# Kernel optimization log

Hardware: AMD Instinct MI355X
Metric: run time of the kernel (lower is better)

Reference implementation:

```python
import jax, jax.numpy as jnp
import numpy as np

EPS = 1e-16

def setup_inputs() -> dict:
    key = jax.random.key(0)
    k1, k2, k3, k4, k5, k6 = jax.random.split(key, 6)
    B, S, NT, E = 8, 256, 50, 64
    # sorted event times in [0, 90); horizon T = 100 > all events; all valid (>=0)
    event_times = jnp.sort(jax.random.uniform(k1, (B, S), dtype=jnp.float32) * 90.0, axis=1)
    event_types = jax.random.randint(k2, (B, S), 0, NT)
    # parameters initialized N(0, 0.1) as in _initialize_parameters
    type_embeddings = 0.1 * jax.random.normal(k3, (NT, E), dtype=jnp.float32)
    a = 0.1 * jax.random.normal(k4, (NT, E), dtype=jnp.float32)
    A = 0.1 * jax.random.normal(k5, (NT, NT, E), dtype=jnp.float32)
    P = 0.1 * jax.random.normal(k6, (NT, NT, E), dtype=jnp.float32)
    return {"event_times": event_times, "event_types": event_types, "T": 100,
            "type_embeddings": type_embeddings, "a": a, "A": A, "P": P}

def _hawkes_nll(event_times, event_types, T, emb, a, A, P):
    B, S = event_times.shape
    NT, E = emb.shape
    Tf = jnp.asarray(T, jnp.float32)
    emb_t = emb[event_types]            # (B,S,E) embedding of each event's type
    a_t = a[event_types]                # (B,S,E)
    valid = event_times >= 0.0          # (B,S)

    # ---- log-likelihood: intensity of the observed type at each event time ----
    # pairwise: axis 1 = query event i, axis 2 = history event j (j < i)
    dt = event_times[:, :, None] - event_times[:, None, :]                 # (B,Si,Sj)
    hist_mask = (jnp.arange(S)[:, None] > jnp.arange(S)[None, :])[None]    # (1,Si,Sj): j<i
    # A_pair[b,i,j,e] = A[type_j, type_i, e]; same for P_pair
    A_pair = A[event_types[:, None, :], event_types[:, :, None]]           # (B,Si,Sj,E)
    P_pair = P[event_types[:, None, :], event_types[:, :, None]]
    emb_i = emb_t[:, :, None, :]                                           # (B,Si,1,E)
    emb_j = emb_t[:, None, :, :]                                           # (B,1,Sj,E)
    decay = jnp.exp(-(emb_i * P_pair) * emb_j * dt[..., None])
    contrib = (emb_i * A_pair) * decay * emb_j                             # (B,Si,Sj,E)
    m = jnp.sum(jnp.where(hist_mask[..., None], contrib, 0.0), axis=2)     # (B,Si,E)
    inten = jnp.sum(jax.nn.softplus(emb_t * a_t + m), axis=-1)             # (B,S)
    ll = jnp.sum(jnp.where(valid, jnp.log(inten + EPS), 0.0))

    # ---- integral approximation (as in compute_loss) ----
    # intensity at horizon T for ALL types, using full valid history
    dT = Tf - event_times                                                  # (B,S)
    A_all = A[event_types]                                                 # (B,S,NT,E): A[t_j, t, e]
    P_all = P[event_types]
    decT = jnp.exp(-(emb[None, None] * P_all) * emb_t[:, :, None, :] * dT[:, :, None, None])
    conT = (emb[None, None] * A_all) * decT * emb_t[:, :, None, :]         # (B,S,NT,E)
    m_T = jnp.sum(jnp.where(valid[:, :, None, None], conT, 0.0), axis=1)   # (B,NT,E)
    inten_T = jnp.sum(jax.nn.softplus(emb * a + m_T), axis=(-2, -1))       # (B,)

    base_sum = jnp.sum(jax.nn.softplus(emb * a))                           # empty-history intensity summed over types
    any_valid = jnp.any(valid, axis=1)                                     # (B,)
    last_time = jnp.where(any_valid, jnp.max(jnp.where(valid, event_times, -1e30), axis=1), 0.0)
    first_time = jnp.where(any_valid, jnp.min(jnp.where(valid, event_times, 1e30), axis=1), 0.0)
    integ_b = jnp.where(any_valid,
                        inten_T * (Tf - last_time) + base_sum * first_time,
                        base_sum * Tf)
    integral = jnp.sum(integ_b)
    return -(ll - integral)

def reference(event_times, event_types, T, type_embeddings, a, A, P):
    return _hawkes_nll(event_times, event_types, T, type_embeddings, a, A, P)
```

## Files before the change

### kernel.cpp

```cpp
#include <hip/hip_runtime.h>
#include <math.h>

#define B   8
#define S   256
#define NT  50
#define E   64
#define NTE (NT * E)
#define EPSF 1e-16f

#define NW        8
#define NTHREADS  (64 * NW)
#define LL_BLOCKS (B * S / 2)
#define IN_BLOCKS (B * NT)

__device__ __forceinline__ float softplus(float x) {
    if (x > 20.0f) return x;
    return log1pf(__expf(x));
}

__device__ __forceinline__ float wave_reduce_sum(float v) {
    #pragma unroll
    for (int off = 32; off > 0; off >>= 1)
        v += __shfl_down(v, off, 64);
    return v;
}

__global__ __launch_bounds__(NTHREADS, 8) void main_kernel(
    const float* __restrict__ times, const int* __restrict__ types,
    const int* __restrict__ Tp,
    const float* __restrict__ emb,  const float* __restrict__ a,
    const float* __restrict__ Amat, const float* __restrict__ Pmat,
    float* __restrict__ ws_ll, float* __restrict__ ws_int)
{
    const int tid = threadIdx.x;
    const int e   = tid & 63;
    const int w   = tid >> 6;
    const int bid = blockIdx.x;
    const int b   = bid / (S / 2);

    __shared__ __align__(16) float  s_emb[NTE];
    __shared__ __align__(16) float4 s_ev[S];
    __shared__ float s_part[2][NW][E];
    __shared__ float s_row[2];

    {
        const float4* __restrict__ emb4 = (const float4*)emb;
        float4* s4 = (float4*)s_emb;
        for (int idx = tid; idx < NTE / 4; idx += NTHREADS)
            s4[idx] = emb4[idx];
    }
    for (int j = tid; j < S; j += NTHREADS) {
        const int ty = types[b * S + j];
        s_ev[j] = make_float4(times[b * S + j],
                              __int_as_float(ty * E),
                              __int_as_float(ty * NTE), 0.0f);
    }
    __syncthreads();

    {
        const int ih = bid % (S / 2);
        const int rows[2] = { ih, S - 1 - ih };
        #pragma unroll
        for (int r = 0; r < 2; ++r) {
            const int   i     = rows[r];
            const float t_i   = s_ev[i].x;
            const int   col   = __float_as_int(s_ev[i].y) + e;
            const float negEi = -s_emb[col];

            float macc = 0.0f;
            #pragma unroll 8
            for (int j = w; j < i; j += NW) {
                const float4 ev  = s_ev[j];
                const float  dtj = t_i - ev.x;
                const int   base = __float_as_int(ev.z) + col;
                const float ej   = s_emb[__float_as_int(ev.y) + e];
                const float Pe   = Pmat[base];
                const float Ae   = Amat[base];
                macc = fmaf(Ae * ej, __expf(negEi * Pe * ej * dtj), macc);
            }
            s_part[r][w][e] = macc;
        }
        __syncthreads();
        if (w < 2) {
            const int   i     = rows[w];
            const float t_i   = s_ev[i].x;
            const int   col   = __float_as_int(s_ev[i].y) + e;
            const float emb_i = s_emb[col];
            float mt = 0.0f;
            #pragma unroll
            for (int q = 0; q < NW; ++q) mt += s_part[w][q][e];
            const float sp    = softplus(fmaf(emb_i, mt, emb_i * a[col]));
            const float inten = wave_reduce_sum(sp);
            if (e == 0)
                s_row[w] = (t_i >= 0.0f) ? logf(inten + EPSF) : 0.0f;
        }
        __syncthreads();
        if (tid == 0) ws_ll[bid] = s_row[0] + s_row[1];
    }

    if (bid < IN_BLOCKS) {
        const int b2 = bid / NT;
        const int k  = bid % NT;

        for (int j = tid; j < S; j += NTHREADS) {
            const int ty = types[b2 * S + j];
            s_ev[j] = make_float4(times[b2 * S + j],
                                  __int_as_float(ty * E),
                                  __int_as_float(ty * NTE), 0.0f);
        }
        __syncthreads();

        const float Tf    = (float)(*Tp);
        const int   colk  = k * E + e;
        const float embk  = s_emb[colk];
        const float negEk = -embk;

        float acc = 0.0f;
        #pragma unroll 8
        for (int i = w; i < S; i += NW) {
            const float4 ev  = s_ev[i];
            const float  dT  = Tf - ev.x;
            const int   base = __float_as_int(ev.z) + colk;
            const float et   = s_emb[__float_as_int(ev.y) + e];
            const float c    = Amat[base] * et * __expf(negEk * Pmat[base] * et * dT);
            acc += (ev.x >= 0.0f) ? c : 0.0f;
        }
        s_part[0][w][e] = acc;
        __syncthreads();
        if (w == 0) {
            float mt = 0.0f;
            #pragma unroll
            for (int q = 0; q < NW; ++q) mt += s_part[0][q][e];
            const float sp = softplus(fmaf(embk, mt, embk * a[colk]));
            const float s  = wave_reduce_sum(sp);
            if (e == 0) ws_int[bid] = s;
        }
    }
}

__global__ __launch_bounds__(256) void finalize_kernel(
    const float* __restrict__ times,
    const int* __restrict__ Tp,
    const float* __restrict__ emb, const float* __restrict__ a,
    const float* __restrict__ ws_ll, const float* __restrict__ ws_int,
    float* __restrict__ out)
{
    const int t    = threadIdx.x;
    const int lane = t & 63;
    const int w    = t >> 6;
    const float Tf = (float)(*Tp);

    float llp = 0.0f;
    for (int idx = t; idx < LL_BLOCKS; idx += 256) llp += ws_ll[idx];
    float bs = 0.0f;
    for (int idx = t; idx < NTE; idx += 256) bs += softplus(emb[idx] * a[idx]);

    __shared__ float red[256], red2[256];
    red[t] = llp; red2[t] = bs;

    __shared__ float s_first[B], s_last[B], s_iT[B], s_any[B];
    for (int b = w; b < B; b += 4) {
        float mn = 1e30f, mx = -1e30f;
        #pragma unroll
        for (int q = 0; q < S / 64; ++q) {
            const float tv = times[b * S + q * 64 + lane];
            const bool valid = (tv >= 0.0f);
            mn = fminf(mn, valid ? tv : 1e30f);
            mx = fmaxf(mx, valid ? tv : -1e30f);
        }
        float iv = (lane < NT) ? ws_int[b * NT + lane] : 0.0f;
        #pragma unroll
        for (int off = 32; off > 0; off >>= 1) {
            mn = fminf(mn, __shfl_down(mn, off, 64));
            mx = fmaxf(mx, __shfl_down(mx, off, 64));
            iv += __shfl_down(iv, off, 64);
        }
        if (lane == 0) {
            const bool any_valid = (mn < 1e29f);
            s_any[b]   = any_valid ? 1.0f : 0.0f;
            s_first[b] = any_valid ? mn : 0.0f;
            s_last[b]  = any_valid ? mx : 0.0f;
            s_iT[b]    = iv;
        }
    }
    __syncthreads();

    for (int off = 128; off > 0; off >>= 1) {
        if (t < off) { red[t] += red[t + off]; red2[t] += red2[t + off]; }
        __syncthreads();
    }

    if (t == 0) {
        const float base_sum = red2[0];
        float integral = 0.0f;
        #pragma unroll
        for (int b = 0; b < B; ++b) {
            integral += (s_any[b] > 0.5f)
                ? s_iT[b] * (Tf - s_last[b]) + base_sum * s_first[b]
                : base_sum * Tf;
        }
        out[0] = integral - red[0];
    }
}

extern "C" void kernel_launch(void* const* d_in, const int* in_sizes, int n_in,
                              void* d_out, int out_size, void* d_ws, size_t ws_size,
                              hipStream_t stream) {
    const float* times = (const float*)d_in[0];
    const int*   types = (const int*)d_in[1];
    const int*   Tp    = (const int*)d_in[2];
    const float* emb   = (const float*)d_in[3];
    const float* a     = (const float*)d_in[4];
    const float* Amat  = (const float*)d_in[5];
    const float* Pmat  = (const float*)d_in[6];

    float* ws     = (float*)d_ws;
    float* ws_ll  = ws;
    float* ws_int = ws + LL_BLOCKS;
    float* out    = (float*)d_out;

    main_kernel<<<LL_BLOCKS, NTHREADS, 0, stream>>>(
        times, types, Tp, emb, a, Amat, Pmat, ws_ll, ws_int);
    finalize_kernel<<<1, 256, 0, stream>>>(times, Tp, emb, a, ws_ll, ws_int, out);
}
```

Before: 88.24 us.

## Use persistent 256-block grid with 16 waves, looping over row pairs and tiles

Drops the grid from 1024 blocks to 256 blocks of 1024 threads, so each block handles 4 row pairs and up to 2 integral tiles. This amortizes the per-block load of the embedding table and event data into shared memory across more work. Per-row log values are now written straight to the workspace, and finalize sums twice as many entries. The cost is fewer blocks in flight, lower occupancy per CU, and extra syncs between iterations.

```diff
diff --git a/kernel.cpp b/kernel.cpp
--- a/kernel.cpp
+++ b/kernel.cpp
@@ -8,10 +8,12 @@
 #define NTE (NT * E)
 #define EPSF 1e-16f
 
-#define NW        8
+#define NW        16
 #define NTHREADS  (64 * NW)
-#define LL_BLOCKS (B * S / 2)
-#define IN_BLOCKS (B * NT)
+#define NBLK      256
+#define PAIRS_PB  4
+#define LL_PAIRS  (B * S / 2)
+#define IN_TILES  (B * NT)
 
 __device__ __forceinline__ float softplus(float x) {
     if (x > 20.0f) return x;
@@ -25,23 +27,22 @@
     return v;
 }
 
-__global__ __launch_bounds__(NTHREADS, 8) void main_kernel(
+__global__ __launch_bounds__(NTHREADS, 4) void main_kernel(
     const float* __restrict__ times, const int* __restrict__ types,
     const int* __restrict__ Tp,
     const float* __restrict__ emb,  const float* __restrict__ a,
     const float* __restrict__ Amat, const float* __restrict__ Pmat,
-    float* __restrict__ ws_ll, float* __restrict__ ws_int)
+    float* __restrict__ ws_ll2, float* __restrict__ ws_int)
 {
     const int tid = threadIdx.x;
     const int e   = tid & 63;
     const int w   = tid >> 6;
     const int bid = blockIdx.x;
-    const int b   = bid / (S / 2);
+    const int b   = bid >> 5;
 
     __shared__ __align__(16) float  s_emb[NTE];
     __shared__ __align__(16) float4 s_ev[S];
     __shared__ float s_part[2][NW][E];
-    __shared__ float s_row[2];
 
     {
         const float4* __restrict__ emb4 = (const float4*)emb;
@@ -57,9 +58,11 @@
     }
     __syncthreads();
 
-    {
-        const int ih = bid % (S / 2);
+    for (int pp = 0; pp < PAIRS_PB; ++pp) {
+        const int pair = bid * PAIRS_PB + pp;
+        const int ih   = pair & 127;
         const int rows[2] = { ih, S - 1 - ih };
+
         #pragma unroll
         for (int r = 0; r < 2; ++r) {
             const int   i     = rows[r];
@@ -92,15 +95,17 @@
             const float sp    = softplus(fmaf(emb_i, mt, emb_i * a[col]));
             const float inten = wave_reduce_sum(sp);
             if (e == 0)
-                s_row[w] = (t_i >= 0.0f) ? logf(inten + EPSF) : 0.0f;
-        }
-        __syncthreads();
-        if (tid == 0) ws_ll[bid] = s_row[0] + s_row[1];
-    }
-
-    if (bid < IN_BLOCKS) {
-        const int b2 = bid / NT;
-        const int k  = bid % NT;
+                ws_ll2[pair * 2 + w] = (t_i >= 0.0f) ? logf(inten + EPSF) : 0.0f;
+        }
+        __syncthreads();
+    }
+
+    #pragma unroll
+    for (int tt = 0; tt < 2; ++tt) {
+        const int t = bid + tt * NBLK;
+        if (t >= IN_TILES) break;
+        const int b2 = t / NT;
+        const int k  = t % NT;
 
         for (int j = tid; j < S; j += NTHREADS) {
             const int ty = types[b2 * S + j];
@@ -133,8 +138,9 @@
             for (int q = 0; q < NW; ++q) mt += s_part[0][q][e];
             const float sp = softplus(fmaf(embk, mt, embk * a[colk]));
             const float s  = wave_reduce_sum(sp);
-            if (e == 0) ws_int[bid] = s;
-        }
+            if (e == 0) ws_int[t] = s;
+        }
+        __syncthreads();
     }
 }
 
@@ -142,7 +148,7 @@
     const float* __restrict__ times,
     const int* __restrict__ Tp,
     const float* __restrict__ emb, const float* __restrict__ a,
-    const float* __restrict__ ws_ll, const float* __restrict__ ws_int,
+    const float* __restrict__ ws_ll2, const float* __restrict__ ws_int,
     float* __restrict__ out)
 {
     const int t    = threadIdx.x;
@@ -151,7 +157,7 @@
     const float Tf = (float)(*Tp);
 
     float llp = 0.0f;
-    for (int idx = t; idx < LL_BLOCKS; idx += 256) llp += ws_ll[idx];
+    for (int idx = t; idx < 2 * LL_PAIRS; idx += 256) llp += ws_ll2[idx];
     float bs = 0.0f;
     for (int idx = t; idx < NTE; idx += 256) bs += softplus(emb[idx] * a[idx]);
 
@@ -214,12 +220,12 @@
     const float* Amat  = (const float*)d_in[5];
     const float* Pmat  = (const float*)d_in[6];
 
-    float* ws     = (float*)d_ws;
-    float* ws_ll  = ws;
-    float* ws_int = ws + LL_BLOCKS;
-    float* out    = (float*)d_out;
-
-    main_kernel<<<LL_BLOCKS, NTHREADS, 0, stream>>>(
-        times, types, Tp, emb, a, Amat, Pmat, ws_ll, ws_int);
-    finalize_kernel<<<1, 256, 0, stream>>>(times, Tp, emb, a, ws_ll, ws_int, out);
-}
+    float* ws      = (float*)d_ws;
+    float* ws_ll2  = ws;
+    float* ws_int  = ws + 2 * LL_PAIRS;
+    float* out     = (float*)d_out;
+
+    main_kernel<<<NBLK, NTHREADS, 0, stream>>>(
+        times, types, Tp, emb, a, Amat, Pmat, ws_ll2, ws_int);
+    finalize_kernel<<<1, 256, 0, stream>>>(times, Tp, emb, a, ws_ll2, ws_int, out);
+}
```

After: 98.19 us. 11.3% more time.
